# Kernel optimization log

Measured on AMD Instinct MI355X. Metric: run time of the kernel, lower is better.

## Reference

```python
import jax, jax.numpy as jnp
import numpy as np

MEAN = np.array([0.485, 0.456, 0.406], np.float32).reshape(1, 3, 1, 1)
STD = np.array([0.229, 0.224, 0.225], np.float32).reshape(1, 3, 1, 1)
BN_EPS = 1e-5


def _srm_kernels():
    """Standard SRM 30-filter 5x5 high-pass bank (Fridrich) -> [30,1,5,5]."""
    ks = []
    Z = lambda: np.zeros((5, 5), np.float32)
    D8 = [(-1, 0), (-1, 1), (0, 1), (1, 1), (1, 0), (1, -1), (0, -1), (-1, -1)]
    for dy, dx in D8:  # 8 first-order
        k = Z(); k[2, 2] = -1.0; k[2 + dy, 2 + dx] = 1.0; ks.append(k)
    for dy, dx in D8[:4]:  # 4 second-order
        k = Z(); k[2, 2] = -2.0; k[2 + dy, 2 + dx] = 1.0; k[2 - dy, 2 - dx] = 1.0
        ks.append(k / 2.0)
    for dy, dx in D8:  # 8 third-order
        k = Z()
        k[2 - dy, 2 - dx] = -1.0; k[2, 2] = 3.0
        k[2 + dy, 2 + dx] = -3.0; k[2 + 2 * dy, 2 + 2 * dx] = 1.0
        ks.append(k / 3.0)
    sq3 = np.array([[-1, 2, -1], [2, -4, 2], [-1, 2, -1]], np.float32) / 4.0
    k = Z(); k[1:4, 1:4] = sq3; ks.append(k)  # SQUARE 3x3
    sq5 = np.array([[-1, 2, -2, 2, -1], [2, -6, 8, -6, 2], [-2, 8, -12, 8, -2],
                    [2, -6, 8, -6, 2], [-1, 2, -2, 2, -1]], np.float32) / 12.0
    ks.append(sq5)  # SQUARE 5x5
    e3 = np.array([[-1, 2, -1], [2, -4, 2], [0, 0, 0]], np.float32) / 4.0
    for r in range(4):  # 4 EDGE 3x3
        k = Z(); k[1:4, 1:4] = np.rot90(e3, r); ks.append(k)
    e5 = np.array([[-1, 2, -2, 2, -1], [2, -6, 8, -6, 2], [-2, 8, -12, 8, -2],
                   [0, 0, 0, 0, 0], [0, 0, 0, 0, 0]], np.float32) / 4.0
    for r in range(4):  # 4 EDGE 5x5
        ks.append(np.rot90(e5, r).copy())
    return np.stack(ks)[:, None]  # [30,1,5,5]

SRM_K = jnp.asarray(_srm_kernels())
GAUSS_K = jnp.asarray((np.outer([1, 4, 6, 4, 1], [1, 4, 6, 4, 1]) / 256.0)
                      .astype(np.float32))[None, None]  # [1,1,5,5]
CFA_K = jnp.asarray((np.array([[0, 1, 0], [1, 0, 1], [0, 1, 0]], np.float32) / 4.0))[None, None]


def conv2d(x, w, b=None):
    y = jax.lax.conv_general_dilated(x, w, (1, 1), 'SAME',
                                     dimension_numbers=('NCHW', 'OIHW', 'NCHW'))
    if b is not None:
        y = y + b[None, :, None, None]
    return y


def batchnorm(x, g, b, m, v):
    inv = jax.lax.rsqrt(v + BN_EPS)
    return (x - m[None, :, None, None]) * (g * inv)[None, :, None, None] + b[None, :, None, None]


def extract_features(x):
    """Batched PRNU(1) + SRM(30) + CFA(1) feature maps -> [B,32,H,W]."""
    img = jnp.clip(x * STD + MEAN, 0.0, 1.0)  # denormalize
    gray = (0.299 * img[:, 0] + 0.587 * img[:, 1] + 0.114 * img[:, 2])[:, None]  # [B,1,H,W]
    prnu = gray - conv2d(gray, GAUSS_K)            # denoise-subtract noise residual
    srm = conv2d(gray, SRM_K)                       # [B,30,H,W]
    green = img[:, 1:2]
    cfa = green - conv2d(green, CFA_K)              # CFA interpolation residual
    return jnp.concatenate([prnu, srm, cfa], axis=1)  # [B,32,H,W]


def setup_inputs() -> dict:
    key = jax.random.key(0)
    ks = jax.random.split(key, 16)
    B, H, W = 16, 256, 256
    d = {"x": jax.random.normal(ks[0], (B, 3, H, W), jnp.float32)}
    cins = [32, 64, 64, 64]
    for i in range(4):
        cin, co = cins[i], 64
        scale = (2.0 / (cin * 9)) ** 0.5  # kaiming
        d[f"w{i+1}"] = jax.random.normal(ks[1 + i], (co, cin, 3, 3), jnp.float32) * scale
        d[f"b{i+1}"] = jnp.zeros((co,), jnp.float32)
        d[f"g{i+1}"] = jnp.ones((co,), jnp.float32)
        d[f"be{i+1}"] = jnp.zeros((co,), jnp.float32)
        d[f"m{i+1}"] = jax.random.normal(ks[5 + i], (co,), jnp.float32) * 0.1
        d[f"v{i+1}"] = jax.random.uniform(ks[9 + i], (co,), jnp.float32, 0.5, 1.5)
    return d


def reference(x, w1, b1, g1, be1, m1, v1, w2, b2, g2, be2, m2, v2,
              w3, b3, g3, be3, m3, v3, w4, b4, g4, be4, m4, v4):
    h = extract_features(x)
    for w, b, g, be, m, v in ((w1, b1, g1, be1, m1, v1), (w2, b2, g2, be2, m2, v2),
                              (w3, b3, g3, be3, m3, v3), (w4, b4, g4, be4, m4, v4)):
        h = jax.nn.relu(batchnorm(conv2d(h, w, b), g, be, m, v))
    return h  # [B,64,H,W]
```

## Files before the change

kernel.cpp:

```cpp
#include <hip/hip_runtime.h>
#include <hip/hip_bf16.h>
#include <cstddef>

#define B_ 16
#define H_ 256
#define W_ 256
#define HW_ (H_ * W_)
#define P_ 258


typedef _Float16 half8 __attribute__((ext_vector_type(8)));
typedef float floatx4 __attribute__((ext_vector_type(4)));

__device__ __forceinline__ void gload_lds16(void* lds, const void* g) {
  __builtin_amdgcn_global_load_lds(
      (const __attribute__((address_space(1))) unsigned int*)g,
      (__attribute__((address_space(3))) unsigned int*)lds, 16, 0, 0);
}

__global__ __launch_bounds__(256) void zero_border3(_Float16* __restrict__ f,
                                                    _Float16* __restrict__ a,
                                                    _Float16* __restrict__ bb) {
  int idx = blockIdx.x * 256 + threadIdx.x;
  int total = 16 * 20 * 1028;
  if (idx >= total) return;
  int p = idx % 1028;
  int rest = idx / 1028;
  int cg = rest % 20;
  int b = rest / 20;
  _Float16* buf;
  int ncg, c;
  if (cg < 4) { buf = f; ncg = 4; c = cg; }
  else if (cg < 12) { buf = a; ncg = 8; c = cg - 4; }
  else { buf = bb; ncg = 8; c = cg - 12; }
  int row, col;
  if (p < 258) { row = 0; col = p; }
  else if (p < 516) { row = 257; col = p - 258; }
  else if (p < 772) { row = p - 515; col = 0; }
  else { row = p - 771; col = 257; }
  *(floatx4*)&buf[(((size_t)(b * ncg + c) * P_ + row) * P_ + col) * 8] =
      (floatx4)0.f;
}

__global__ __launch_bounds__(256) void feat_kernel(const float* __restrict__ x,
                                                   _Float16* __restrict__ F) {
  __shared__ float sg[36][37];
  __shared__ float sgr[36][37];

  const int b = blockIdx.z;
  const int y0 = blockIdx.y * 32;
  const int x0 = blockIdx.x * 32;
  const float* xb = x + (size_t)b * 3 * HW_;

  for (int i = threadIdx.x; i < 36 * 36; i += 256) {
    int iy = i / 36, ix = i % 36;
    int gy = y0 + iy - 2, gx = x0 + ix - 2;
    float gray = 0.f, green = 0.f;
    if (gy >= 0 && gy < H_ && gx >= 0 && gx < W_) {
      int idx = gy * W_ + gx;
      float r = fminf(fmaxf(xb[idx] * 0.229f + 0.485f, 0.f), 1.f);
      float g = fminf(fmaxf(xb[idx + HW_] * 0.224f + 0.456f, 0.f), 1.f);
      float bl = fminf(fmaxf(xb[idx + 2 * HW_] * 0.225f + 0.406f, 0.f), 1.f);
      gray = 0.299f * r + 0.587f * g + 0.114f * bl;
      green = g;
    }
    sg[iy][ix] = gray;
    sgr[iy][ix] = green;
  }
  __syncthreads();

  for (int p = threadIdx.x; p < 32 * 32; p += 256) {
    const int py = p >> 5, px = p & 31;
    const int ly = py + 2, lx = px + 2;
#define G(dy, dx) sg[ly + (dy)][lx + (dx)]
    float f[32];
    const float c = G(0, 0);

    {
      const float ga[5] = {1.f, 4.f, 6.f, 4.f, 1.f};
      float s = 0.f;
#pragma unroll
      for (int i = 0; i < 5; i++) {
        float rs = 0.f;
#pragma unroll
        for (int j = 0; j < 5; j++) rs += ga[j] * G(i - 2, j - 2);
        s += ga[i] * rs;
      }
      f[0] = c - s * (1.0f / 256.0f);
    }

    const int dy8[8] = {-1, -1, 0, 1, 1, 1, 0, -1};
    const int dx8[8] = {0, 1, 1, 1, 0, -1, -1, -1};

#pragma unroll
    for (int k = 0; k < 8; k++) f[1 + k] = G(dy8[k], dx8[k]) - c;
#pragma unroll
    for (int k = 0; k < 4; k++)
      f[9 + k] = 0.5f * (G(dy8[k], dx8[k]) + G(-dy8[k], -dx8[k])) - c;
#pragma unroll
    for (int k = 0; k < 8; k++)
      f[13 + k] = (-G(-dy8[k], -dx8[k]) + 3.f * c - 3.f * G(dy8[k], dx8[k]) +
                   G(2 * dy8[k], 2 * dx8[k])) * (1.f / 3.f);

    {
      const float sq3[3][3] = {{-1, 2, -1}, {2, -4, 2}, {-1, 2, -1}};
      float s = 0.f;
#pragma unroll
      for (int i = 0; i < 3; i++)
#pragma unroll
        for (int j = 0; j < 3; j++) s += sq3[i][j] * G(i - 1, j - 1);
      f[21] = s * 0.25f;
    }
    {
      const float sq5[5][5] = {{-1, 2, -2, 2, -1},
                               {2, -6, 8, -6, 2},
                               {-2, 8, -12, 8, -2},
                               {2, -6, 8, -6, 2},
                               {-1, 2, -2, 2, -1}};
      float s = 0.f;
#pragma unroll
      for (int i = 0; i < 5; i++)
#pragma unroll
        for (int j = 0; j < 5; j++) s += sq5[i][j] * G(i - 2, j - 2);
      f[22] = s * (1.0f / 12.0f);
    }
    {
      const float e3[3][3] = {{-1, 2, -1}, {2, -4, 2}, {0, 0, 0}};
      float s0 = 0.f, s1 = 0.f, s2 = 0.f, s3 = 0.f;
#pragma unroll
      for (int i = 0; i < 3; i++)
#pragma unroll
        for (int j = 0; j < 3; j++) {
          float v = G(i - 1, j - 1);
          s0 += e3[i][j] * v;
          s1 += e3[j][2 - i] * v;
          s2 += e3[2 - i][2 - j] * v;
          s3 += e3[2 - j][i] * v;
        }
      f[23] = s0 * 0.25f;
      f[24] = s1 * 0.25f;
      f[25] = s2 * 0.25f;
      f[26] = s3 * 0.25f;
    }
    {
      const float e5[5][5] = {{-1, 2, -2, 2, -1},
                              {2, -6, 8, -6, 2},
                              {-2, 8, -12, 8, -2},
                              {0, 0, 0, 0, 0},
                              {0, 0, 0, 0, 0}};
      float s0 = 0.f, s1 = 0.f, s2 = 0.f, s3 = 0.f;
#pragma unroll
      for (int i = 0; i < 5; i++)
#pragma unroll
        for (int j = 0; j < 5; j++) {
          float v = G(i - 2, j - 2);
          s0 += e5[i][j] * v;
          s1 += e5[j][4 - i] * v;
          s2 += e5[4 - i][4 - j] * v;
          s3 += e5[4 - j][i] * v;
        }
      f[27] = s0 * 0.25f;
      f[28] = s1 * 0.25f;
      f[29] = s2 * 0.25f;
      f[30] = s3 * 0.25f;
    }
    {
      float gc = sgr[ly][lx];
      f[31] = gc - 0.25f * (sgr[ly - 1][lx] + sgr[ly][lx - 1] +
                            sgr[ly][lx + 1] + sgr[ly + 1][lx]);
    }
#undef G

    _Float16 h[32];
#pragma unroll
    for (int cc = 0; cc < 32; cc++) h[cc] = (_Float16)f[cc];
    const floatx4* src = (const floatx4*)h;
#pragma unroll
    for (int cg = 0; cg < 4; cg++)
      *(floatx4*)&F[(((size_t)(b * 4 + cg) * P_ + (y0 + py + 1)) * P_ +
                     (x0 + px + 1)) * 8] = src[cg];
  }
}

__global__ void wprep4_kernel(
    const float* __restrict__ w1, const float* __restrict__ b1,
    const float* __restrict__ g1, const float* __restrict__ be1,
    const float* __restrict__ m1, const float* __restrict__ v1,
    const float* __restrict__ w2, const float* __restrict__ b2,
    const float* __restrict__ g2, const float* __restrict__ be2,
    const float* __restrict__ m2, const float* __restrict__ v2,
    const float* __restrict__ w3, const float* __restrict__ b3,
    const float* __restrict__ g3, const float* __restrict__ be3,
    const float* __restrict__ m3, const float* __restrict__ v3,
    const float* __restrict__ w4, const float* __restrict__ b4,
    const float* __restrict__ g4, const float* __restrict__ be4,
    const float* __restrict__ m4, const float* __restrict__ v4,
    _Float16* __restrict__ wp1, _Float16* __restrict__ wp2,
    _Float16* __restrict__ wp3, _Float16* __restrict__ wp4,
    float* __restrict__ scsh) {
  const int layer = blockIdx.y;
  const float *w, *bias, *g, *be, *m, *v;
  _Float16* wp;
  int cin;
  switch (layer) {
    case 0: w = w1; bias = b1; g = g1; be = be1; m = m1; v = v1; wp = wp1; cin = 32; break;
    case 1: w = w2; bias = b2; g = g2; be = be2; m = m2; v = v2; wp = wp2; cin = 64; break;
    case 2: w = w3; bias = b3; g = g3; be = be3; m = m3; v = v3; wp = wp3; cin = 64; break;
    default: w = w4; bias = b4; g = g4; be = be4; m = m4; v = v4; wp = wp4; cin = 64; break;
  }
  int i = blockIdx.x * 256 + threadIdx.x;
  int total = cin * 9 * 64;
  if (i < total) {
    int j = i & 7;
    int co = (i >> 3) & 63;
    int rest = i >> 9;
    int t = rest % 9;
    int qc = rest / 9;
    int ci = qc * 8 + j;
    wp[i] = (_Float16)w[((size_t)co * cin + ci) * 9 + t];
  }
  if (i < 64) {
    float s = g[i] * rsqrtf(v[i] + 1e-5f);
    scsh[layer * 128 + i] = s;
    scsh[layer * 128 + 64 + i] = be[i] + (bias[i] - m[i]) * s;
  }
}

template <int CIN, bool FINAL>
__global__ __launch_bounds__(256, CIN == 32 ? 2 : 1) void conv_mfma(
    const _Float16* __restrict__ in, const _Float16* __restrict__ wp,
    const float* __restrict__ sc, const float* __restrict__ sh,
    void* __restrict__ outv) {
  constexpr int NP = CIN / 8;
  constexpr int IN_BYTES = NP * 10 * 66 * 8 * 2;
  constexpr int W_BYTES = NP * 9 * 64 * 8 * 2;
  constexpr int IN_UNITS = NP * 10 * 66;
  constexpr int W_UNITS = W_BYTES / 16;

  __shared__ char smem[IN_BYTES + W_BYTES];
  _Float16(*s_in)[10][66][8] = (_Float16(*)[10][66][8])smem;
  _Float16(*s_w)[9][64][8] = (_Float16(*)[9][64][8])(smem + IN_BYTES);

  const int tid = threadIdx.x;
  const int b = blockIdx.z;
  const int y0 = blockIdx.y * 8;
  const int x0 = blockIdx.x * 64;
  const int wid = tid >> 6;
  const int lane = tid & 63;
  const int quad = lane >> 4;
  const int ln = lane & 15;

  floatx4 acc[8][4];
#pragma unroll
  for (int mt = 0; mt < 8; mt++)
#pragma unroll
    for (int nt = 0; nt < 4; nt++) acc[mt][nt] = (floatx4)0.f;

  for (int i = tid; i < IN_UNITS; i += 256) {
    int q = i / 660, rem = i % 660;
    int row = rem / 66, col = rem % 66;
    gload_lds16(smem + i * 16,
                &in[(((size_t)(b * NP + q) * P_ + (y0 + row)) * P_ +
                     (x0 + col)) * 8]);
  }
  for (int i = tid; i < W_UNITS; i += 256) {
    gload_lds16(smem + IN_BYTES + i * 16, wp + (size_t)i * 8);
  }
  __syncthreads();

  for (int kc = 0; kc < NP / 4; kc++) {
#pragma unroll
    for (int t = 0; t < 9; t++) {
      const int ty = t / 3, tx = t % 3;
      half8 a[8], bb[4];
#pragma unroll
      for (int nt = 0; nt < 4; nt++)
        bb[nt] = *(const half8*)&s_w[kc * 4 + quad][t][nt * 16 + ln][0];
#pragma unroll
      for (int mt = 0; mt < 8; mt++)
        a[mt] = *(const half8*)&s_in[kc * 4 + quad]
                                    [2 * wid + ty + (mt >> 2)]
                                    [(mt & 3) * 16 + ln + tx][0];
#pragma unroll
      for (int mt = 0; mt < 8; mt++)
#pragma unroll
        for (int nt = 0; nt < 4; nt++)
          acc[mt][nt] = __builtin_amdgcn_mfma_f32_16x16x32_f16(
              a[mt], bb[nt], acc[mt][nt], 0, 0, 0);
    }
  }

  if (FINAL) {
    float* out = (float*)outv;
#pragma unroll
    for (int nt = 0; nt < 4; nt++) {
      int co = nt * 16 + ln;
      float s = sc[co], t0 = sh[co];
#pragma unroll
      for (int mt = 0; mt < 8; mt++) {
        int y = y0 + 2 * wid + (mt >> 2);
        int xb = x0 + (mt & 3) * 16 + quad * 4;
        floatx4 vv;
#pragma unroll
        for (int r = 0; r < 4; r++) vv[r] = fmaxf(acc[mt][nt][r] * s + t0, 0.f);
        *(floatx4*)&out[(((size_t)b * 64 + co) * H_ + y) * W_ + xb] = vv;
      }
    }
  } else {
    __syncthreads();
    _Float16* s_out = (_Float16*)smem + wid * 8192;
#pragma unroll
    for (int nt = 0; nt < 4; nt++) {
      int co = nt * 16 + ln;
      float s = sc[co], t0 = sh[co];
      int cog = co >> 3, clo = co & 7;
#pragma unroll
      for (int mt = 0; mt < 8; mt++) {
        int pix0 = (mt >> 2) * 64 + (mt & 3) * 16 + quad * 4;
#pragma unroll
        for (int r = 0; r < 4; r++) {
          int pix = pix0 + r;
          s_out[pix * 64 + (((cog ^ (pix & 7)) << 3) | clo)] =
              (_Float16)fmaxf(acc[mt][nt][r] * s + t0, 0.f);
        }
      }
    }
    __builtin_amdgcn_s_waitcnt(0);
    _Float16* out = (_Float16*)outv;
#pragma unroll
    for (int k = 0; k < 16; k++) {
      int rw = k >> 3, cog = k & 7;
      int pix = rw * 64 + lane;
      int gy = y0 + 2 * wid + rw + 1, gx = x0 + lane + 1;
      *(floatx4*)&out[(((size_t)(b * 8 + cog) * P_ + gy) * P_ + gx) * 8] =
          *(const floatx4*)&s_out[pix * 64 + ((cog ^ (lane & 7)) << 3)];
    }
  }
}

extern "C" void kernel_launch(void* const* d_in, const int* in_sizes, int n_in,
                              void* d_out, int out_size, void* d_ws,
                              size_t ws_size, hipStream_t stream) {
  const float* x = (const float*)d_in[0];
#define LAYER_PTRS(i)                                                       \
  const float* w##i = (const float*)d_in[1 + ((i)-1) * 6 + 0];              \
  const float* b##i = (const float*)d_in[1 + ((i)-1) * 6 + 1];              \
  const float* g##i = (const float*)d_in[1 + ((i)-1) * 6 + 2];              \
  const float* be##i = (const float*)d_in[1 + ((i)-1) * 6 + 3];             \
  const float* m##i = (const float*)d_in[1 + ((i)-1) * 6 + 4];              \
  const float* v##i = (const float*)d_in[1 + ((i)-1) * 6 + 5];
  LAYER_PTRS(1)
  LAYER_PTRS(2)
  LAYER_PTRS(3)
  LAYER_PTRS(4)
#undef LAYER_PTRS

  char* ws = (char*)d_ws;
  const size_t featB = (size_t)16 * 4 * P_ * P_ * 8 * 2;
  const size_t actB64 = (size_t)16 * 8 * P_ * P_ * 8 * 2;
  _Float16* feat = (_Float16*)ws;
  _Float16* actA = (_Float16*)(ws + featB);
  _Float16* actB = (_Float16*)(ws + featB + actB64);
  char* wbase = ws + featB + 2 * actB64;
  _Float16* wp1 = (_Float16*)(wbase);
  _Float16* wp2 = (_Float16*)(wbase + 36864);
  _Float16* wp3 = (_Float16*)(wbase + 36864 + 73728);
  _Float16* wp4 = (_Float16*)(wbase + 36864 + 2 * 73728);
  float* scsh = (float*)(wbase + 36864 + 3 * 73728);
  float *sc1 = scsh, *sh1 = scsh + 64;
  float *sc2 = scsh + 128, *sh2 = scsh + 192;
  float *sc3 = scsh + 256, *sh3 = scsh + 320;
  float *sc4 = scsh + 384, *sh4 = scsh + 448;

  dim3 wgrid(144, 4);
  wprep4_kernel<<<wgrid, 256, 0, stream>>>(
      w1, b1, g1, be1, m1, v1, w2, b2, g2, be2, m2, v2,
      w3, b3, g3, be3, m3, v3, w4, b4, g4, be4, m4, v4,
      wp1, wp2, wp3, wp4, scsh);

  zero_border3<<<1285, 256, 0, stream>>>(feat, actA, actB);

  dim3 fgrid(W_ / 32, H_ / 32, B_);
  feat_kernel<<<fgrid, 256, 0, stream>>>(x, feat);

  dim3 cgrid(W_ / 64, H_ / 8, B_);
  conv_mfma<32, false><<<cgrid, 256, 0, stream>>>(feat, wp1, sc1, sh1, actA);
  conv_mfma<64, false><<<cgrid, 256, 0, stream>>>(actA, wp2, sc2, sh2, actB);
  conv_mfma<64, false><<<cgrid, 256, 0, stream>>>(actB, wp3, sc3, sh3, actA);
  conv_mfma<64, true><<<cgrid, 256, 0, stream>>>(actA, wp4, sc4, sh4, d_out);
}
```

Baseline: 739.7 us.

## Chunk input channels through fixed LDS, read weights from global for occupancy 2

After: 696.9 us. 1.06x faster.

```diff
diff --git a/kernel.cpp b/kernel.cpp
--- a/kernel.cpp
+++ b/kernel.cpp
@@ -227,19 +227,12 @@
 }
 
 template <int CIN, bool FINAL>
-__global__ __launch_bounds__(256, CIN == 32 ? 2 : 1) void conv_mfma(
+__global__ __launch_bounds__(256, 2) void conv_mfma(
     const _Float16* __restrict__ in, const _Float16* __restrict__ wp,
     const float* __restrict__ sc, const float* __restrict__ sh,
     void* __restrict__ outv) {
-  constexpr int NP = CIN / 8;
-  constexpr int IN_BYTES = NP * 10 * 66 * 8 * 2;
-  constexpr int W_BYTES = NP * 9 * 64 * 8 * 2;
-  constexpr int IN_UNITS = NP * 10 * 66;
-  constexpr int W_UNITS = W_BYTES / 16;
-
-  __shared__ char smem[IN_BYTES + W_BYTES];
+  __shared__ char smem[42240];
   _Float16(*s_in)[10][66][8] = (_Float16(*)[10][66][8])smem;
-  _Float16(*s_w)[9][64][8] = (_Float16(*)[9][64][8])(smem + IN_BYTES);
 
   const int tid = threadIdx.x;
   const int b = blockIdx.z;
@@ -256,30 +249,28 @@
 #pragma unroll
     for (int nt = 0; nt < 4; nt++) acc[mt][nt] = (floatx4)0.f;
 
-  for (int i = tid; i < IN_UNITS; i += 256) {
-    int q = i / 660, rem = i % 660;
-    int row = rem / 66, col = rem % 66;
-    gload_lds16(smem + i * 16,
-                &in[(((size_t)(b * NP + q) * P_ + (y0 + row)) * P_ +
-                     (x0 + col)) * 8]);
-  }
-  for (int i = tid; i < W_UNITS; i += 256) {
-    gload_lds16(smem + IN_BYTES + i * 16, wp + (size_t)i * 8);
-  }
-  __syncthreads();
-
-  for (int kc = 0; kc < NP / 4; kc++) {
+  for (int kc = 0; kc < CIN / 32; kc++) {
+    __syncthreads();
+    for (int i = tid; i < 2640; i += 256) {
+      int q = i / 660, rem = i % 660;
+      int row = rem / 66, col = rem % 66;
+      gload_lds16(smem + i * 16,
+                  &in[(((size_t)(b * (CIN / 8) + kc * 4 + q) * P_ +
+                        (y0 + row)) * P_ + (x0 + col)) * 8]);
+    }
+    __syncthreads();
+
+    const _Float16* wq = wp + (size_t)(kc * 4 + quad) * 9 * 512;
 #pragma unroll
     for (int t = 0; t < 9; t++) {
       const int ty = t / 3, tx = t % 3;
       half8 a[8], bb[4];
 #pragma unroll
       for (int nt = 0; nt < 4; nt++)
-        bb[nt] = *(const half8*)&s_w[kc * 4 + quad][t][nt * 16 + ln][0];
+        bb[nt] = *(const half8*)&wq[t * 512 + (nt * 16 + ln) * 8];
 #pragma unroll
       for (int mt = 0; mt < 8; mt++)
-        a[mt] = *(const half8*)&s_in[kc * 4 + quad]
-                                    [2 * wid + ty + (mt >> 2)]
+        a[mt] = *(const half8*)&s_in[quad][2 * wid + ty + (mt >> 2)]
                                     [(mt & 3) * 16 + ln + tx][0];
 #pragma unroll
       for (int mt = 0; mt < 8; mt++)
@@ -308,32 +299,35 @@
     }
   } else {
     __syncthreads();
-    _Float16* s_out = (_Float16*)smem + wid * 8192;
-#pragma unroll
-    for (int nt = 0; nt < 4; nt++) {
-      int co = nt * 16 + ln;
-      float s = sc[co], t0 = sh[co];
-      int cog = co >> 3, clo = co & 7;
-#pragma unroll
-      for (int mt = 0; mt < 8; mt++) {
-        int pix0 = (mt >> 2) * 64 + (mt & 3) * 16 + quad * 4;
-#pragma unroll
-        for (int r = 0; r < 4; r++) {
-          int pix = pix0 + r;
-          s_out[pix * 64 + (((cog ^ (pix & 7)) << 3) | clo)] =
-              (_Float16)fmaxf(acc[mt][nt][r] * s + t0, 0.f);
+    _Float16* s_out = (_Float16*)smem + wid * 5280;
+    _Float16* out = (_Float16*)outv;
+#pragma unroll
+    for (int h = 0; h < 2; h++) {
+      asm volatile("s_waitcnt lgkmcnt(0)" ::: "memory");
+#pragma unroll
+      for (int nt = 0; nt < 4; nt++) {
+        int co = nt * 16 + ln;
+        float s = sc[co], t0 = sh[co];
+        int cog = co >> 3, clo = co & 7;
+#pragma unroll
+        for (int mt2 = 0; mt2 < 4; mt2++) {
+          int lpix0 = mt2 * 16 + quad * 4;
+#pragma unroll
+          for (int r = 0; r < 4; r++) {
+            int lpix = lpix0 + r;
+            s_out[lpix * 64 + (((cog ^ (lpix & 7)) << 3) | clo)] =
+                (_Float16)fmaxf(acc[h * 4 + mt2][nt][r] * s + t0, 0.f);
+          }
         }
       }
-    }
-    __builtin_amdgcn_s_waitcnt(0);
-    _Float16* out = (_Float16*)outv;
-#pragma unroll
-    for (int k = 0; k < 16; k++) {
-      int rw = k >> 3, cog = k & 7;
-      int pix = rw * 64 + lane;
-      int gy = y0 + 2 * wid + rw + 1, gx = x0 + lane + 1;
-      *(floatx4*)&out[(((size_t)(b * 8 + cog) * P_ + gy) * P_ + gx) * 8] =
-          *(const floatx4*)&s_out[pix * 64 + ((cog ^ (lane & 7)) << 3)];
+      asm volatile("s_waitcnt lgkmcnt(0)" ::: "memory");
+      int gy = y0 + 2 * wid + h + 1;
+#pragma unroll
+      for (int cog = 0; cog < 8; cog++) {
+        *(floatx4*)&out[(((size_t)(b * 8 + cog) * P_ + gy) * P_ +
+                         (x0 + lane + 1)) * 8] =
+            *(const floatx4*)&s_out[lane * 64 + ((cog ^ (lane & 7)) << 3)];
+      }
     }
   }
 }
```

## Chunk conv input channels through fixed LDS to raise occupancy and swizzle block order

Applied to the files above, without the earlier changes.

Result: faster. 624.6 us (-15.6%).

```diff
diff --git a/kernel.cpp b/kernel.cpp
--- a/kernel.cpp
+++ b/kernel.cpp
@@ -227,24 +227,21 @@
 }
 
 template <int CIN, bool FINAL>
-__global__ __launch_bounds__(256, CIN == 32 ? 2 : 1) void conv_mfma(
+__global__ __launch_bounds__(256, 2) void conv_mfma(
     const _Float16* __restrict__ in, const _Float16* __restrict__ wp,
     const float* __restrict__ sc, const float* __restrict__ sh,
     void* __restrict__ outv) {
-  constexpr int NP = CIN / 8;
-  constexpr int IN_BYTES = NP * 10 * 66 * 8 * 2;
-  constexpr int W_BYTES = NP * 9 * 64 * 8 * 2;
-  constexpr int IN_UNITS = NP * 10 * 66;
-  constexpr int W_UNITS = W_BYTES / 16;
-
-  __shared__ char smem[IN_BYTES + W_BYTES];
+  __shared__ char smem[42240 + 36864];
   _Float16(*s_in)[10][66][8] = (_Float16(*)[10][66][8])smem;
-  _Float16(*s_w)[9][64][8] = (_Float16(*)[9][64][8])(smem + IN_BYTES);
+  _Float16(*s_w)[9][64][8] = (_Float16(*)[9][64][8])(smem + 42240);
+
+  const int bid = blockIdx.x;
+  const int sid = (bid & 7) * 256 + (bid >> 3);
+  const int b = sid >> 7;
+  const int y0 = ((sid >> 2) & 31) * 8;
+  const int x0 = (sid & 3) * 64;
 
   const int tid = threadIdx.x;
-  const int b = blockIdx.z;
-  const int y0 = blockIdx.y * 8;
-  const int x0 = blockIdx.x * 64;
   const int wid = tid >> 6;
   const int lane = tid & 63;
   const int quad = lane >> 4;
@@ -256,31 +253,31 @@
 #pragma unroll
     for (int nt = 0; nt < 4; nt++) acc[mt][nt] = (floatx4)0.f;
 
-  for (int i = tid; i < IN_UNITS; i += 256) {
-    int q = i / 660, rem = i % 660;
-    int row = rem / 66, col = rem % 66;
-    gload_lds16(smem + i * 16,
-                &in[(((size_t)(b * NP + q) * P_ + (y0 + row)) * P_ +
-                     (x0 + col)) * 8]);
-  }
-  for (int i = tid; i < W_UNITS; i += 256) {
-    gload_lds16(smem + IN_BYTES + i * 16, wp + (size_t)i * 8);
-  }
-  __syncthreads();
-
-  for (int kc = 0; kc < NP / 4; kc++) {
+  for (int kc = 0; kc < CIN / 32; kc++) {
+    __syncthreads();
+    for (int i = tid; i < 2640; i += 256) {
+      int q = i / 660, rem = i % 660;
+      int row = rem / 66, col = rem % 66;
+      gload_lds16(smem + i * 16,
+                  &in[(((size_t)(b * (CIN / 8) + kc * 4 + q) * P_ +
+                        (y0 + row)) * P_ + (x0 + col)) * 8]);
+    }
+    for (int i = tid; i < 2304; i += 256) {
+      gload_lds16(smem + 42240 + i * 16, wp + ((size_t)kc * 2304 + i) * 8);
+    }
+    __syncthreads();
+
 #pragma unroll
     for (int t = 0; t < 9; t++) {
       const int ty = t / 3, tx = t % 3;
       half8 a[8], bb[4];
 #pragma unroll
       for (int nt = 0; nt < 4; nt++)
-        bb[nt] = *(const half8*)&s_w[kc * 4 + quad][t][nt * 16 + ln][0];
+        bb[nt] = *(const half8*)&s_w[quad][t][nt * 16 + ln][0];
 #pragma unroll
       for (int mt = 0; mt < 8; mt++)
-        a[mt] = *(const half8*)&s_in[kc * 4 + quad]
-                                    [2 * wid + ty + (mt >> 2)]
-                                    [(mt & 3) * 16 + ln + tx][0];
+        a[mt] = *(const half8*)
+            &s_in[quad][2 * wid + ty + (mt >> 2)][(mt & 3) * 16 + ln + tx][0];
 #pragma unroll
       for (int mt = 0; mt < 8; mt++)
 #pragma unroll
@@ -325,7 +322,7 @@
         }
       }
     }
-    __builtin_amdgcn_s_waitcnt(0);
+    asm volatile("s_waitcnt lgkmcnt(0)" ::: "memory");
     _Float16* out = (_Float16*)outv;
 #pragma unroll
     for (int k = 0; k < 16; k++) {
@@ -383,9 +380,8 @@
   dim3 fgrid(W_ / 32, H_ / 32, B_);
   feat_kernel<<<fgrid, 256, 0, stream>>>(x, feat);
 
-  dim3 cgrid(W_ / 64, H_ / 8, B_);
-  conv_mfma<32, false><<<cgrid, 256, 0, stream>>>(feat, wp1, sc1, sh1, actA);
-  conv_mfma<64, false><<<cgrid, 256, 0, stream>>>(actA, wp2, sc2, sh2, actB);
-  conv_mfma<64, false><<<cgrid, 256, 0, stream>>>(actB, wp3, sc3, sh3, actA);
-  conv_mfma<64, true><<<cgrid, 256, 0, stream>>>(actA, wp4, sc4, sh4, d_out);
-}
+  conv_mfma<32, false><<<2048, 256, 0, stream>>>(feat, wp1, sc1, sh1, actA);
+  conv_mfma<64, false><<<2048, 256, 0, stream>>>(actA, wp2, sc2, sh2, actB);
+  conv_mfma<64, false><<<2048, 256, 0, stream>>>(actB, wp3, sc3, sh3, actA);
+  conv_mfma<64, true><<<2048, 256, 0, stream>>>(actA, wp4, sc4, sh4, d_out);
+}
```
